# Kernel tuning notes

Measured on AMD Instinct MI355X. Metric: run time of the kernel, lower is better.

Reference implementation:

```python
import jax, jax.numpy as jnp
import numpy as np

BATCH_SIZE = 4096
N_VIEWS = 2
NUM_GPU = 1
TEMPERATURE = 0.07
FEAT_DIM = 128
N = (BATCH_SIZE // NUM_GPU) * N_VIEWS  # 8192


def setup_inputs() -> dict:
    key = jax.random.key(0)
    features = jax.random.normal(key, (N, FEAT_DIM), dtype=jnp.float32)
    return {"features": features}


def reference(features):
    n = features.shape[0]
    b = BATCH_SIZE // NUM_GPU
    # labels: [arange(b)] * n_views concatenated -> pairwise equality matrix
    lbl_vec = jnp.tile(jnp.arange(b), N_VIEWS)            # [N]
    lab = lbl_vec[None, :] == lbl_vec[:, None]            # [N, N] bool

    # F.normalize(dim=1): divide by L2 norm clamped at 1e-12
    norm = jnp.linalg.norm(features, axis=1, keepdims=True)
    f = features / jnp.maximum(norm, 1e-12)
    sim = f @ f.T                                          # [N, N]

    # Remove diagonal: row i keeps columns j != i in original order.
    cols = jnp.arange(n - 1)
    off_idx = cols[None, :] + (cols[None, :] >= jnp.arange(n)[:, None])  # [N, N-1]
    sim_od = jnp.take_along_axis(sim, off_idx, axis=1)     # [N, N-1]
    lab_od = jnp.take_along_axis(lab, off_idx, axis=1)     # [N, N-1] bool

    # Stable sort: positives (label True) first, preserving original column order,
    # matching torch's masked-select + concat([positives, negatives]).
    order = jnp.argsort(~lab_od, axis=1, stable=True)      # [N, N-1]
    logits = jnp.take_along_axis(sim_od, order, axis=1) / TEMPERATURE

    # CrossEntropyLoss with target class 0 (mean reduction)
    loss = -jax.nn.log_softmax(logits, axis=1)[:, 0]
    return loss.mean()
```

## Files before the change

kernel.cpp:

```cpp
#include <hip/hip_runtime.h>
#include <hip/hip_bf16.h>
#include <cstdint>

#define NROWS 8192
#define FDIM  128
#define HALF_N 4096

typedef short bf16x8 __attribute__((ext_vector_type(8)));
typedef float f32x4  __attribute__((ext_vector_type(4)));

#define K1 (1.4426950408889634f / 0.07f)

#if __has_builtin(__builtin_amdgcn_exp2f)
#define EXP2(x) __builtin_amdgcn_exp2f(x)
#else
#define EXP2(x) exp2f(x)
#endif


__global__ void __launch_bounds__(256) normalize_kernel(const float* __restrict__ f,
                                                        short* __restrict__ packed,
                                                        float* __restrict__ esum_g) {
    const int row  = blockIdx.x * 4 + (threadIdx.x >> 6);
    const int lane = threadIdx.x & 63;
    const float2 v = ((const float2*)(f + (size_t)row * FDIM))[lane];
    float ss = v.x * v.x + v.y * v.y;
    #pragma unroll
    for (int m = 1; m < 64; m <<= 1) ss += __shfl_xor(ss, m);
    const float scale = 1.0f / fmaxf(sqrtf(ss), 1e-12f);

    const int off = ((((row >> 4) * 4 + (lane >> 4)) * 64)
                     + ((lane >> 2) & 3) * 16 + (row & 15)) * 8 + 2 * (lane & 3);
    __hip_bfloat16 b0 = __float2bfloat16(v.x * scale);
    __hip_bfloat16 b1 = __float2bfloat16(v.y * scale);
    unsigned u = (unsigned)*(unsigned short*)&b0
               | ((unsigned)*(unsigned short*)&b1 << 16);
    *(unsigned*)(packed + off) = u;

    if (threadIdx.x < 4) esum_g[blockIdx.x * 4 + threadIdx.x] = 0.0f;
}

__device__ __forceinline__ float2 bf2_to_f2(unsigned u) {
    return make_float2(__uint_as_float(u << 16),
                       __uint_as_float(u & 0xffff0000u));
}

__global__ void __launch_bounds__(256, 4) sim_kernel(const short* __restrict__ pk,
                                                     float* __restrict__ esum_g,
                                                     float* __restrict__ pos_g,
                                                     float* __restrict__ diag_g) {
    if (blockIdx.x >= 1024) {
        const int i  = (blockIdx.x - 1024) * 256 + threadIdx.x;
        const int ip = i ^ HALF_N;
        const uint4* P = (const uint4*)pk;
        float dot = 0.f, self = 0.f;
        #pragma unroll
        for (int cc = 0; cc < 16; cc++) {
            const uint4 a = P[((i  >> 4) * 4 + (cc >> 2)) * 64 + (cc & 3) * 16 + (i  & 15)];
            const uint4 b = P[((ip >> 4) * 4 + (cc >> 2)) * 64 + (cc & 3) * 16 + (ip & 15)];
            const unsigned au[4] = {a.x, a.y, a.z, a.w};
            const unsigned bu[4] = {b.x, b.y, b.z, b.w};
            #pragma unroll
            for (int q = 0; q < 4; q++) {
                const float2 av = bf2_to_f2(au[q]);
                const float2 bv = bf2_to_f2(bu[q]);
                dot  = __builtin_fmaf(av.x, bv.x, __builtin_fmaf(av.y, bv.y, dot));
                self = __builtin_fmaf(av.x, av.x, __builtin_fmaf(av.y, av.y, self));
            }
        }
        pos_g[i]  = dot;
        diag_g[i] = EXP2(__builtin_fmaf(self, K1, -K1));
        return;
    }

    const int tid   = threadIdx.x;
    const int w     = tid >> 6;
    const int lane  = tid & 63;
    const int quad  = lane >> 4;
    const int l16   = lane & 15;
    const int j     = blockIdx.x & 15;
    const int strip = (blockIdx.x >> 4) * 4 + w;
    const bf16x8* P = (const bf16x8*)pk;

    bf16x8 a_reg[4][2];
    #pragma unroll
    for (int fr = 0; fr < 2; fr++)
        #pragma unroll
        for (int ks = 0; ks < 4; ks++)
            a_reg[ks][fr] = P[(((strip * 2 + fr) * 4) + ks) * 64 + lane];

    float ep[2][4];
    #pragma unroll
    for (int a = 0; a < 2; a++)
        #pragma unroll
        for (int b = 0; b < 4; b++) ep[a][b] = 0.0f;

    const int cb0 = j * 32;

    #pragma unroll 8
    for (int cb = 0; cb < 32; cb++) {
        bf16x8 b[4];
        #pragma unroll
        for (int ks = 0; ks < 4; ks++)
            b[ks] = P[((cb0 + cb) * 4 + ks) * 64 + lane];

        f32x4 acc[2];
        #pragma unroll
        for (int fr = 0; fr < 2; fr++) acc[fr] = (f32x4){0.f, 0.f, 0.f, 0.f};
        #pragma unroll
        for (int ks = 0; ks < 4; ks++)
            #pragma unroll
            for (int fr = 0; fr < 2; fr++)
                acc[fr] = __builtin_amdgcn_mfma_f32_16x16x32_bf16(
                              a_reg[ks][fr], b[ks], acc[fr], 0, 0, 0);

        #pragma unroll
        for (int fr = 0; fr < 2; fr++)
            #pragma unroll
            for (int r = 0; r < 4; r++)
                ep[fr][r] += EXP2(__builtin_fmaf(acc[fr][r], K1, -K1));
    }

    #pragma unroll
    for (int fr = 0; fr < 2; fr++)
        #pragma unroll
        for (int r = 0; r < 4; r++) {
            float v = ep[fr][r];
            #pragma unroll
            for (int m = 1; m < 16; m <<= 1) v += __shfl_xor(v, m);
            if (l16 == 0)
                atomicAdd(&esum_g[strip * 32 + fr * 16 + quad * 4 + r], v);
        }
}

__global__ void __launch_bounds__(256) final_kernel(const float* __restrict__ esum_g,
                                                    const float* __restrict__ pos_g,
                                                    const float* __restrict__ diag_g,
                                                    float* __restrict__ out) {
    const int tid = threadIdx.x;
    const float invT = 1.0f / 0.07f;
    float acc = 0.0f;
    for (int i = tid; i < NROWS; i += 256)
        acc += logf(esum_g[i] - diag_g[i]) + invT - pos_g[i] * invT;
    #pragma unroll
    for (int m = 1; m < 64; m <<= 1) acc += __shfl_xor(acc, m);
    __shared__ float ws[4];
    if ((tid & 63) == 0) ws[tid >> 6] = acc;
    __syncthreads();
    if (tid == 0) out[0] = (ws[0] + ws[1] + ws[2] + ws[3]) * (1.0f / (float)NROWS);
}

extern "C" void kernel_launch(void* const* d_in, const int* in_sizes, int n_in,
                              void* d_out, int out_size, void* d_ws, size_t ws_size,
                              hipStream_t stream) {
    const float* features = (const float*)d_in[0];
    float* out = (float*)d_out;

    char* ws = (char*)d_ws;
    short* packed = (short*)ws;
    float* esum_g = (float*)(ws + 2097152);
    float* pos_g  = (float*)(ws + 2097152 + 32768);
    float* diag_g = (float*)(ws + 2097152 + 65536);

    normalize_kernel<<<NROWS / 4, 256, 0, stream>>>(features, packed, esum_g);

    sim_kernel<<<1024 + NROWS / 256, 256, 0, stream>>>(packed, esum_g, pos_g, diag_g);

    final_kernel<<<1, 256, 0, stream>>>(esum_g, pos_g, diag_g, out);
}
```

Measured before the change: 89.56 us.

## Exploit symmetry of similarity matrix by computing only upper-triangular tiles

Remaps the GEMM grid to a triangular tile schedule so each off-diagonal 256x256 tile of the symmetric similarity matrix is computed once. Its exp values feed both the row sums and, through a shared-memory column reduction, the transposed row sums. This is meant to roughly halve the MFMA and exp work. It adds per-iteration shuffles, LDS atomics and extra global atomics, and makes diagonal and off-diagonal blocks carry uneven work.

```diff
diff --git a/kernel.cpp b/kernel.cpp
--- a/kernel.cpp
+++ b/kernel.cpp
@@ -16,6 +16,8 @@
 #else
 #define EXP2(x) exp2f(x)
 #endif
+
+#define NBLK_TRI 1056
 
 
 __global__ void __launch_bounds__(256) normalize_kernel(const float* __restrict__ f,
@@ -49,8 +51,8 @@
                                                      float* __restrict__ esum_g,
                                                      float* __restrict__ pos_g,
                                                      float* __restrict__ diag_g) {
-    if (blockIdx.x >= 1024) {
-        const int i  = (blockIdx.x - 1024) * 256 + threadIdx.x;
+    if (blockIdx.x >= NBLK_TRI) {
+        const int i  = (blockIdx.x - NBLK_TRI) * 256 + threadIdx.x;
         const int ip = i ^ HALF_N;
         const uint4* P = (const uint4*)pk;
         float dot = 0.f, self = 0.f;
@@ -73,14 +75,23 @@
         return;
     }
 
+    const int t = blockIdx.x;
+    int J = (int)((sqrtf(4.0f * (float)t + 1.0f) - 1.0f) * 0.5f);
+    while ((J + 1) * (J + 2) <= t) J++;
+    while (J * (J + 1) > t) J--;
+    const int rb = t - J * (J + 1);
+    const bool upper = rb < 2 * J;
+
     const int tid   = threadIdx.x;
     const int w     = tid >> 6;
     const int lane  = tid & 63;
     const int quad  = lane >> 4;
     const int l16   = lane & 15;
-    const int j     = blockIdx.x & 15;
-    const int strip = (blockIdx.x >> 4) * 4 + w;
+    const int strip = rb * 4 + w;
     const bf16x8* P = (const bf16x8*)pk;
+
+    __shared__ float colsum[256];
+    colsum[tid] = 0.0f;
 
     bf16x8 a_reg[4][2];
     #pragma unroll
@@ -95,10 +106,12 @@
         #pragma unroll
         for (int b = 0; b < 4; b++) ep[a][b] = 0.0f;
 
-    const int cb0 = j * 32;
+    __syncthreads();
+
+    const int cb0 = J * 16;
 
     #pragma unroll 8
-    for (int cb = 0; cb < 32; cb++) {
+    for (int cb = 0; cb < 16; cb++) {
         bf16x8 b[4];
         #pragma unroll
         for (int ks = 0; ks < 4; ks++)
@@ -114,11 +127,22 @@
                 acc[fr] = __builtin_amdgcn_mfma_f32_16x16x32_bf16(
                               a_reg[ks][fr], b[ks], acc[fr], 0, 0, 0);
 
+        float cs = 0.0f;
         #pragma unroll
         for (int fr = 0; fr < 2; fr++)
             #pragma unroll
-            for (int r = 0; r < 4; r++)
-                ep[fr][r] += EXP2(__builtin_fmaf(acc[fr][r], K1, -K1));
+            for (int r = 0; r < 4; r++) {
+                const float e = EXP2(__builtin_fmaf(acc[fr][r], K1, -K1));
+                ep[fr][r] += e;
+                cs += e;
+            }
+
+        if (upper) {
+            cs += __shfl_xor(cs, 16);
+            cs += __shfl_xor(cs, 32);
+            if (quad == 0)
+                atomicAdd(&colsum[cb * 16 + l16], cs);
+        }
     }
 
     #pragma unroll
@@ -131,6 +155,9 @@
             if (l16 == 0)
                 atomicAdd(&esum_g[strip * 32 + fr * 16 + quad * 4 + r], v);
         }
+
+    __syncthreads();
+    if (upper) atomicAdd(&esum_g[J * 256 + tid], colsum[tid]);
 }
 
 __global__ void __launch_bounds__(256) final_kernel(const float* __restrict__ esum_g,
@@ -164,7 +191,7 @@
 
     normalize_kernel<<<NROWS / 4, 256, 0, stream>>>(features, packed, esum_g);
 
-    sim_kernel<<<1024 + NROWS / 256, 256, 0, stream>>>(packed, esum_g, pos_g, diag_g);
+    sim_kernel<<<NBLK_TRI + NROWS / 256, 256, 0, stream>>>(packed, esum_g, pos_g, diag_g);
 
     final_kernel<<<1, 256, 0, stream>>>(esum_g, pos_g, diag_g, out);
 }
```

New measurement: 92.71 us. +3.5%, slower.
